# Optimization experiments

Hardware: AMD Instinct MI355X
Metric: run time of the kernel (lower is better)

Reference implementation:

```python
import jax, jax.numpy as jnp
import numpy as np

N_NODES, N_EDGES, N_CRYS = 50000, 1200000, 256
AF, NF, NR = 64, 64, 16
INV_SQRT_2 = 1.0 / 2.0 ** 0.5
EPS = 1e-5


def crystal_norm(x, idx, nseg, gamma, beta):
    # per-crystal, per-feature mean/var normalization
    cnt = jnp.maximum(jax.ops.segment_sum(jnp.ones((x.shape[0],), x.dtype), idx, nseg), 1.0)[:, None]
    mean = jax.ops.segment_sum(x, idx, nseg) / cnt
    d = x - mean[idx]
    var = jax.ops.segment_sum(d * d, idx, nseg) / cnt
    return d / jnp.sqrt(var[idx] + EPS) * gamma + beta


def setup_inputs() -> dict:
    key = jax.random.key(0)
    ks = jax.random.split(key, 16)
    s = 0.05
    return {
        'atom_fea': jax.random.normal(ks[0], (N_NODES, AF), jnp.float32),
        'edge': jax.random.normal(ks[1], (N_EDGES, NF), jnp.float32),
        'rbf': jax.random.uniform(ks[2], (N_EDGES, NR), jnp.float32),
        'nbr_fea_idx': jax.random.randint(ks[3], (N_EDGES, 2), 0, N_NODES),
        'crystal_atom_idx': jax.random.randint(ks[4], (N_NODES,), 0, N_CRYS),
        'crystal_edge_idx': jax.random.randint(ks[5], (N_EDGES,), 0, N_CRYS),
        'W_rbf': jax.random.normal(ks[6], (NR, NF), jnp.float32) * s,
        'W_full': jax.random.normal(ks[7], (2 * AF + NF, 2 * AF), jnp.float32) * s,
        'W_mask': jax.random.normal(ks[8], (AF, 1), jnp.float32) * s,
        'g1': jnp.ones((2 * AF,), jnp.float32),
        'b1': jnp.zeros((2 * AF,), jnp.float32),
        'g2': jnp.ones((AF,), jnp.float32),
        'b2': jnp.zeros((AF,), jnp.float32),
        'Wr1a': jax.random.normal(ks[9], (AF, AF // 2), jnp.float32) * s,
        'Wr1b': jax.random.normal(ks[10], (AF // 2, AF), jnp.float32) * s,
        'Wr2a': jax.random.normal(ks[11], (AF, AF // 2), jnp.float32) * s,
        'Wr2b': jax.random.normal(ks[12], (AF // 2, AF), jnp.float32) * s,
    }


def reference(atom_fea, edge, rbf, nbr_fea_idx, crystal_atom_idx, crystal_edge_idx,
              W_rbf, W_full, W_mask, g1, b1, g2, b2, Wr1a, Wr1b, Wr2a, Wr2b):
    rbf_h = rbf @ W_rbf                                   # [E, NF]
    sum_idx = nbr_fea_idx[:, 0]
    nbr_fea = edge * rbf_h                                # [E, NF]
    atom_nbr_fea = atom_fea[nbr_fea_idx].reshape(-1, 2 * AF)  # [E, 2*AF]
    total = jnp.concatenate([atom_nbr_fea, nbr_fea], axis=1)  # [E, 2*AF+NF]
    gated = total @ W_full                                # [E, 2*AF]
    gated = crystal_norm(gated, crystal_edge_idx, N_CRYS, g1, b1)
    nbr_filter, nbr_core = gated[:, :AF], gated[:, AF:]
    nbr_filter = jax.nn.sigmoid(nbr_filter @ W_mask)      # [E, 1]
    nbr_core = jax.nn.relu(nbr_core)
    msg = nbr_filter * nbr_core                           # [E, AF]
    cnt = jnp.maximum(jax.ops.segment_sum(jnp.ones((msg.shape[0],), msg.dtype), sum_idx, N_NODES), 1.0)[:, None]
    nbr_sumed = jax.ops.segment_sum(msg, sum_idx, N_NODES) / cnt  # scatter-mean
    nbr_sumed = crystal_norm(nbr_sumed, crystal_atom_idx, N_CRYS, g2, b2)
    # 2 residual blocks: out = (x + relu(relu(x W_a) W_b)) / sqrt(2)
    h = jax.nn.relu(jax.nn.relu(nbr_sumed @ Wr1a) @ Wr1b)
    nbr_sumed = (nbr_sumed + h) * INV_SQRT_2
    h = jax.nn.relu(jax.nn.relu(nbr_sumed @ Wr2a) @ Wr2b)
    nbr_sumed = (nbr_sumed + h) * INV_SQRT_2
    return INV_SQRT_2 * jax.nn.relu(atom_fea + nbr_sumed)
```

## Files before the change

### kernel.cpp

```cpp
#include <hip/hip_runtime.h>
#include <hip/hip_bf16.h>

typedef __attribute__((ext_vector_type(8))) short bfrag;
typedef __attribute__((ext_vector_type(4))) float f4;

__device__ __forceinline__ unsigned short f2bf(float f){
  unsigned b = __float_as_uint(f);
  b = (b + 0x7fffu + ((b >> 16) & 1u)) >> 16;
  return (unsigned short)b;
}
__device__ __forceinline__ unsigned pk2bf(float a, float b){
  return (unsigned)f2bf(a) | ((unsigned)f2bf(b) << 16);
}
__device__ __forceinline__ float bf2f(unsigned short u){
  return __uint_as_float(((unsigned)u) << 16);
}
__device__ __forceinline__ bfrag pack8(float4 x, float4 y){
  bfrag r;
  r[0]=(short)f2bf(x.x); r[1]=(short)f2bf(x.y); r[2]=(short)f2bf(x.z); r[3]=(short)f2bf(x.w);
  r[4]=(short)f2bf(y.x); r[5]=(short)f2bf(y.y); r[6]=(short)f2bf(y.z); r[7]=(short)f2bf(y.w);
  return r;
}

__global__ __launch_bounds__(64) void k_prep(const float* __restrict__ Wf, unsigned short* __restrict__ Bpack){
  int l = threadIdx.x; int f = blockIdx.x; int ks = f >> 3; int nt = f & 7;
  int kg = l >> 4; int nn = l & 15;
#pragma unroll
  for (int j = 0; j < 8; ++j){
    int k;
    if (ks < 4) k = ks*32 + kg*8 + j;
    else        k = 128 + (ks-4)*32 + ((j>>2)<<4) + kg*4 + (j&3);
    Bpack[((size_t)f*64 + l)*8 + j] = f2bf(Wf[(size_t)k*128 + nt*16 + nn]);
  }
}

__global__ __launch_bounds__(256) void k_pre(const int* __restrict__ cidxe, int E,
                                             const int* __restrict__ cidxn, int NN,
                                             const int* __restrict__ nbr,
                                             int* __restrict__ ccnte, int* __restrict__ ccntn,
                                             int* __restrict__ ncnt){
  __shared__ int he[256], hn[256];
  int t = threadIdx.x;
  he[t] = 0; hn[t] = 0;
  __syncthreads();
  for (size_t i = (size_t)blockIdx.x*256 + t; i < (size_t)E; i += (size_t)gridDim.x*256){
    atomicAdd(&he[cidxe[i]], 1);
    atomicAdd(&ncnt[nbr[2*i]], 1);
  }
  for (size_t i = (size_t)blockIdx.x*256 + t; i < (size_t)NN; i += (size_t)gridDim.x*256)
    atomicAdd(&hn[cidxn[i]], 1);
  __syncthreads();
  if (he[t]) atomicAdd(&ccnte[t], he[t]);
  if (hn[t]) atomicAdd(&ccntn[t], hn[t]);
}

__global__ __launch_bounds__(1024) void k_scans(const int* __restrict__ ncnt, int NN,
                                                int* __restrict__ offs, int* __restrict__ cursor,
                                                const int* __restrict__ ccnte, const int* __restrict__ ccntn,
                                                int* __restrict__ ceoffs, int* __restrict__ cecur,
                                                int* __restrict__ cnoffs, int* __restrict__ cncur){
  int tid = threadIdx.x;
  if (blockIdx.x == 0){
    __shared__ int part[1024];
    int chunk = (NN + 1023) >> 10;
    int base = tid*chunk;
    int s = 0;
    for (int i = 0; i < chunk; ++i){ int p = base + i; if (p < NN) s += ncnt[p]; }
    part[tid] = s;
    __syncthreads();
    for (int d = 1; d < 1024; d <<= 1){
      int v = (tid >= d) ? part[tid - d] : 0;
      __syncthreads();
      part[tid] += v;
      __syncthreads();
    }
    int run = (tid == 0) ? 0 : part[tid-1];
    for (int i = 0; i < chunk; ++i){
      int p = base + i;
      if (p < NN){ offs[p] = run; cursor[p] = run; run += ncnt[p]; }
    }
    if (tid == 1023) offs[NN] = part[1023];
  } else {
    __shared__ int sh[256];
    const int* cnt = (blockIdx.x == 2) ? ccntn : ccnte;
    int* off = (blockIdx.x == 2) ? cnoffs : ceoffs;
    int* cur = (blockIdx.x == 2) ? cncur  : cecur;
    int v = 0;
    if (tid < 256){ v = cnt[tid]; sh[tid] = v; }
    __syncthreads();
    for (int d = 1; d < 256; d <<= 1){
      int x = (tid >= d && tid < 256) ? sh[tid - d] : 0;
      __syncthreads();
      if (tid < 256) sh[tid] += x;
      __syncthreads();
    }
    if (tid < 256){
      off[tid] = sh[tid] - v; cur[tid] = sh[tid] - v;
      if (tid == 255) off[256] = sh[255];
    }
  }
}

__global__ __launch_bounds__(256) void k_scatter2(const int* __restrict__ nbr, const int* __restrict__ cidxe,
                                                  int E, int* __restrict__ cursor, int4* __restrict__ edat,
                                                  int* __restrict__ gcur, int* __restrict__ celist){
  __shared__ int lhist[256], lbase[256], lcur[256];
  int t = threadIdx.x;
  lhist[t] = 0; lcur[t] = 0;
  __syncthreads();
  int base = blockIdx.x*1024;
  int end = min(base + 1024, E);
  for (int i = base + t; i < end; i += 256) atomicAdd(&lhist[cidxe[i]], 1);
  __syncthreads();
  if (lhist[t]) lbase[t] = atomicAdd(&gcur[t], lhist[t]);
  __syncthreads();
  for (int i = base + t; i < end; i += 256){
    int cr = cidxe[i];
    int n = nbr[2*(size_t)i];
    int j = nbr[2*(size_t)i + 1];
    int pos = atomicAdd(&cursor[n], 1);
    edat[pos] = make_int4(n, j, i, cr);
    int lp = atomicAdd(&lcur[cr], 1);
    celist[lbase[cr] + lp] = pos;
  }
}

__global__ __launch_bounds__(256) void k_cscatter(const int* __restrict__ idx, int n,
                                                  int* __restrict__ gcur, int* __restrict__ outl){
  __shared__ int lhist[256], lbase[256], lcur[256];
  int t = threadIdx.x;
  lhist[t] = 0; lcur[t] = 0;
  __syncthreads();
  int base = blockIdx.x*4096;
  int end = min(base + 4096, n);
  for (int i = base + t; i < end; i += 256) atomicAdd(&lhist[idx[i]], 1);
  __syncthreads();
  if (lhist[t]) lbase[t] = atomicAdd(&gcur[t], lhist[t]);
  __syncthreads();
  for (int i = base + t; i < end; i += 256){
    int b = idx[i];
    int p = atomicAdd(&lcur[b], 1);
    outl[lbase[b] + p] = i;
  }
}

struct TileRegs {
  int ei;
  float4 ra0, ra1, rb0, rb1, rc0, rc1, rd0, rd1, rr0, rr1, re0, re1, re2, re3;
};

__device__ __forceinline__ TileRegs load_tile(const float* __restrict__ atom, const float* __restrict__ edgef,
                                              const float* __restrict__ rbff, const int4* __restrict__ edat,
                                              size_t r0, int e16, int g, int E){
  TileRegs R;
  size_t er = r0 + e16;
  if (er >= (size_t)E) er = 0;
  const int4 ed = edat[er];
  R.ei = ed.z;
  const float4* Ai = (const float4*)(atom + (size_t)ed.x*64);
  const float4* Aj = (const float4*)(atom + (size_t)ed.y*64);
  R.ra0 = Ai[g*2];   R.ra1 = Ai[g*2+1];
  R.rb0 = Ai[8+g*2]; R.rb1 = Ai[8+g*2+1];
  R.rc0 = Aj[g*2];   R.rc1 = Aj[g*2+1];
  R.rd0 = Aj[8+g*2]; R.rd1 = Aj[8+g*2+1];
  R.rr0 = make_float4(0.f,0.f,0.f,0.f);
  R.rr1 = make_float4(0.f,0.f,0.f,0.f);
  if (g < 2){
    const float4* rp = (const float4*)(rbff + (size_t)ed.z*16 + g*8);
    R.rr0 = rp[0]; R.rr1 = rp[1];
  }
  const float4* ep = (const float4*)(edgef + (size_t)ed.z*64);
  R.re0 = ep[g]; R.re1 = ep[4+g]; R.re2 = ep[8+g]; R.re3 = ep[12+g];
  return R;
}

template<int FNT0, int FNT1>
__global__ __launch_bounds__(256) void k_gemm(const float* __restrict__ atom, const float* __restrict__ edgef,
                                              const float* __restrict__ rbff, const int4* __restrict__ edat,
                                              const float* __restrict__ Wrbf,
                                              const unsigned short* __restrict__ Bpack,
                                              unsigned short* __restrict__ gated, int gstride, int colOff,
                                              int nT, int E)
{
  const int lane = threadIdx.x & 63;
  const int wid  = (blockIdx.x*256 + threadIdx.x) >> 6;
  const int nW   = gridDim.x*4;
  const int e16  = lane & 15;
  const int g    = lane >> 4;
  const f4 zero = {0.f, 0.f, 0.f, 0.f};

  bfrag wf[4];
#pragma unroll
  for (int ct = 0; ct < 4; ++ct){
#pragma unroll
    for (int i = 0; i < 8; ++i){
      float v = (g < 2) ? Wrbf[(g*8 + i)*64 + ct*16 + e16] : 0.f;
      wf[ct][i] = (short)f2bf(v);
    }
  }

  size_t t = (size_t)wid;
  if (t >= (size_t)nT) return;
  TileRegs cur = load_tile(atom, edgef, rbff, edat, t*16, e16, g, E);

  while (true){
    const size_t tn = t + (size_t)nW;
    const bool more = tn < (size_t)nT;
    TileRegs nxt;
    if (more) nxt = load_tile(atom, edgef, rbff, edat, tn*16, e16, g, E);

    const size_t r0 = t*16;
    size_t er = r0 + e16;
    const bool rowOK = er < (size_t)E;
    if (!rowOK) er = 0;

    bfrag a[6];
    a[0] = pack8(cur.ra0, cur.ra1);
    a[1] = pack8(cur.rb0, cur.rb1);
    a[2] = pack8(cur.rc0, cur.rc1);
    a[3] = pack8(cur.rd0, cur.rd1);
    bfrag rf = pack8(cur.rr0, cur.rr1);

    f4 h0 = __builtin_amdgcn_mfma_f32_16x16x32_bf16(wf[0], rf, zero, 0, 0, 0);
    f4 h1 = __builtin_amdgcn_mfma_f32_16x16x32_bf16(wf[1], rf, zero, 0, 0, 0);
    f4 h2 = __builtin_amdgcn_mfma_f32_16x16x32_bf16(wf[2], rf, zero, 0, 0, 0);
    f4 h3 = __builtin_amdgcn_mfma_f32_16x16x32_bf16(wf[3], rf, zero, 0, 0, 0);

    const float* pe0 = (const float*)&cur.re0;
    const float* pe1 = (const float*)&cur.re1;
    const float* pe2 = (const float*)&cur.re2;
    const float* pe3 = (const float*)&cur.re3;
#pragma unroll
    for (int r = 0; r < 4; ++r){
      a[4][r]   = (short)f2bf(h0[r]*pe0[r]);
      a[4][4+r] = (short)f2bf(h1[r]*pe1[r]);
      a[5][r]   = (short)f2bf(h2[r]*pe2[r]);
      a[5][4+r] = (short)f2bf(h3[r]*pe3[r]);
    }

    unsigned short* orow = gated + er*(size_t)gstride - colOff;
#pragma unroll
    for (int f_nt = FNT0; f_nt < FNT1; ++f_nt){
      const unsigned short* bb = Bpack + ((size_t)(f_nt*64 + lane))*8;
      f4 acc = zero;
#pragma unroll
      for (int ks = 0; ks < 6; ++ks){
        bfrag b = *(const bfrag*)(bb + (size_t)ks*4096);
        acc = __builtin_amdgcn_mfma_f32_16x16x32_bf16(b, a[ks], acc, 0, 0, 0);
      }
      if (rowOK){
        uint2 pk;
        pk.x = pk2bf(acc[0], acc[1]);
        pk.y = pk2bf(acc[2], acc[3]);
        *(uint2*)(orow + f_nt*16 + g*4) = pk;
      }
    }

    if (!more) break;
    cur = nxt;
    t = tn;
  }
}

__global__ __launch_bounds__(256) void k_cstats128(const unsigned short* __restrict__ gated,
                                                   const int* __restrict__ coffs, const int* __restrict__ celist,
                                                   float* __restrict__ pstat){
  int cr = blockIdx.x >> 3, s = blockIdx.x & 7;
  int t = threadIdx.x, w = t >> 6, lane = t & 63;
  int o0 = coffs[cr], o1 = coffs[cr+1];
  long long L = o1 - o0;
  int lo = o0 + (int)(L*s/8), hi = o0 + (int)(L*(s+1)/8);
  float S0=0.f, Q0=0.f, S1=0.f, Q1=0.f;
  for (int p = lo + w*8; p < hi; p += 32){
#pragma unroll
    for (int u = 0; u < 8; ++u){
      if (p + u < hi){
        int e = celist[p+u];
        unsigned v = *(const unsigned*)(gated + (size_t)e*128 + lane*2);
        float a = bf2f((unsigned short)(v & 0xffffu));
        float b = bf2f((unsigned short)(v >> 16));
        S0 += a; Q0 += a*a; S1 += b; Q1 += b*b;
      }
    }
  }
  __shared__ float sP[4][256];
  sP[w][lane*4+0]=S0; sP[w][lane*4+1]=Q0; sP[w][lane*4+2]=S1; sP[w][lane*4+3]=Q1;
  __syncthreads();
  float v = sP[0][t] + sP[1][t] + sP[2][t] + sP[3][t];
  pstat[((size_t)blockIdx.x << 8) + t] = v;
}

__global__ __launch_bounds__(256) void k_cstats64(const unsigned short* __restrict__ gated,
                                                  const int* __restrict__ coffs, const int* __restrict__ celist,
                                                  float* __restrict__ pstat){
  int cr = blockIdx.x >> 3, s = blockIdx.x & 7;
  int t = threadIdx.x, w = t >> 6, lane = t & 63;
  int o0 = coffs[cr], o1 = coffs[cr+1];
  long long L = o1 - o0;
  int lo = o0 + (int)(L*s/8), hi = o0 + (int)(L*(s+1)/8);
  float S=0.f, Q=0.f;
  for (int p = lo + w*8; p < hi; p += 32){
#pragma unroll
    for (int u = 0; u < 8; ++u){
      if (p + u < hi){
        int e = celist[p+u];
        float a = bf2f(gated[(size_t)e*64 + lane]);
        S += a; Q += a*a;
      }
    }
  }
  __shared__ float sP[4][128];
  sP[w][lane*2+0]=S; sP[w][lane*2+1]=Q;
  __syncthreads();
  if (t < 128){
    float v = sP[0][t] + sP[1][t] + sP[2][t] + sP[3][t];
    pstat[((size_t)blockIdx.x << 7) + t] = v;
  }
}

__global__ __launch_bounds__(256) void k_cnstats(const float* __restrict__ nacc, const int* __restrict__ ncnt,
                                                 const int* __restrict__ coffs, const int* __restrict__ cnlist,
                                                 float* __restrict__ pstat){
  int cr = blockIdx.x >> 1, s = blockIdx.x & 1;
  int t = threadIdx.x, w = t >> 6, lane = t & 63;
  int o0 = coffs[cr], o1 = coffs[cr+1];
  long long L = o1 - o0;
  int lo = o0 + (int)(L*s/2), hi = o0 + (int)(L*(s+1)/2);
  float S=0.f, Q=0.f;
  for (int p = lo + w*4; p < hi; p += 16){
#pragma unroll
    for (int u = 0; u < 4; ++u){
      if (p + u < hi){
        int n = cnlist[p+u];
        float inv = 1.f / fmaxf((float)ncnt[n], 1.f);
        float a = nacc[(size_t)n*64 + lane]*inv;
        S += a; Q += a*a;
      }
    }
  }
  __shared__ float sP[4][128];
  sP[w][lane*2+0]=S; sP[w][lane*2+1]=Q;
  __syncthreads();
  if (t < 128){
    float v = sP[0][t] + sP[1][t] + sP[2][t] + sP[3][t];
    pstat[((size_t)blockIdx.x << 7) + t] = v;
  }
}

__global__ __launch_bounds__(256) void k_red128f(const float* __restrict__ pstat, const int* __restrict__ ccnt,
                                                 const float* __restrict__ gamma, const float* __restrict__ beta,
                                                 const float* __restrict__ Wm,
                                                 float* __restrict__ sc, float* __restrict__ sh,
                                                 float* __restrict__ w2, float* __restrict__ fb){
  int idx = blockIdx.x*256 + threadIdx.x;
  int cr = idx >> 7, col = idx & 127;
  int vS = ((col >> 1) << 2) + ((col & 1) << 1);
  float S=0.f, Q=0.f;
  for (int s2 = 0; s2 < 8; ++s2){
    const float* b = pstat + ((size_t)(cr*8 + s2) << 8);
    S += b[vS]; Q += b[vS+1];
  }
  float cnt = fmaxf((float)ccnt[cr], 1.f);
  float mean = S/cnt;
  float var = fmaxf(Q/cnt - mean*mean, 0.f);
  float r = 1.f / sqrtf(var + 1e-5f);
  float g = r*gamma[col];
  float shv = beta[col] - mean*g;
  sc[cr*128 + col] = g;
  sh[cr*128 + col] = shv;

  __shared__ float red[256];
  float contrib = 0.f;
  if (col < 64){
    float wmv = Wm[col];
    w2[cr*64 + col] = g*wmv;
    contrib = shv*wmv;
  }
  red[threadIdx.x] = contrib;
  __syncthreads();
  int lc = threadIdx.x & 127;
  for (int d = 32; d > 0; d >>= 1){
    if (lc < d) red[threadIdx.x] += red[threadIdx.x + d];
    __syncthreads();
  }
  if (lc == 0) fb[cr] = red[threadIdx.x];
}

__global__ __launch_bounds__(256) void k_red64(const float* __restrict__ pstat, int nsplit,
                                               const int* __restrict__ ccnt,
                                               const float* __restrict__ gamma, const float* __restrict__ beta,
                                               float* __restrict__ sc, float* __restrict__ sh,
                                               int stride, int colOff){
  int idx = blockIdx.x*256 + threadIdx.x;
  int cr = idx >> 6, col = idx & 63;
  int vS = col*2;
  float S=0.f, Q=0.f;
  for (int s2 = 0; s2 < nsplit; ++s2){
    const float* b = pstat + ((size_t)(cr*nsplit + s2) << 7);
    S += b[vS]; Q += b[vS+1];
  }
  float cnt = fmaxf((float)ccnt[cr], 1.f);
  float mean = S/cnt;
  float var = fmaxf(Q/cnt - mean*mean, 0.f);
  float r = 1.f / sqrtf(var + 1e-5f);
  float g = r*gamma[col];
  sc[cr*stride + colOff + col] = g;
  sh[cr*stride + colOff + col] = beta[col] - mean*g;
}

__global__ __launch_bounds__(256) void k_fprep(const float* __restrict__ scE, const float* __restrict__ shE,
                                               const float* __restrict__ Wm, float* __restrict__ w2,
                                               float* __restrict__ fb){
  int t = threadIdx.x, w = t >> 6, lane = t & 63;
  int cr = blockIdx.x*4 + w;
  float wm = Wm[lane];
  w2[cr*64 + lane] = scE[cr*128 + lane]*wm;
  float b = shE[cr*128 + lane]*wm;
#pragma unroll
  for (int d = 1; d < 64; d <<= 1) b += __shfl_xor(b, d, 64);
  if (lane == 0) fb[cr] = b;
}

__global__ __launch_bounds__(256) void k_filter(const unsigned short* __restrict__ gated, int gst,
                                                const int4* __restrict__ edat, const float* __restrict__ w2,
                                                const float* __restrict__ fb, float* __restrict__ filt, int E){
  size_t r = (size_t)blockIdx.x*256 + threadIdx.x;
  if (r >= (size_t)E) return;
  int cr = edat[r].w;
  const uint4* row = (const uint4*)(gated + r*(size_t)gst);
  const float4* wr = (const float4*)(w2 + cr*64);
  float logit = fb[cr];
#pragma unroll
  for (int j = 0; j < 8; ++j){
    uint4 v = row[j];
    float4 wa = wr[2*j], wb = wr[2*j+1];
    logit += bf2f((unsigned short)(v.x & 0xffffu))*wa.x + bf2f((unsigned short)(v.x >> 16))*wa.y;
    logit += bf2f((unsigned short)(v.y & 0xffffu))*wa.z + bf2f((unsigned short)(v.y >> 16))*wa.w;
    logit += bf2f((unsigned short)(v.z & 0xffffu))*wb.x + bf2f((unsigned short)(v.z >> 16))*wb.y;
    logit += bf2f((unsigned short)(v.w & 0xffffu))*wb.z + bf2f((unsigned short)(v.w >> 16))*wb.w;
  }
  filt[r] = 1.f / (1.f + __expf(-logit));
}

__global__ __launch_bounds__(256) void k_msgf8(const unsigned short* __restrict__ gated,
                                               const int4* __restrict__ edat,
                                               const int* __restrict__ offs,
                                               const float* __restrict__ scE, const float* __restrict__ shE,
                                               const float* __restrict__ w2, const float* __restrict__ fb,
                                               float* __restrict__ nacc, int NN){
  int w = threadIdx.x >> 6, lane = threadIdx.x & 63;
  int n = blockIdx.x*4 + w;
  if (n >= NN) return;
  int sub = lane >> 3, c8 = lane & 7;
  float a0=0.f,a1=0.f,a2=0.f,a3=0.f,a4=0.f,a5=0.f,a6=0.f,a7=0.f;
  int p0 = offs[n], p1 = offs[n+1];
  for (int p = p0; p < p1; p += 8){
    int q = p + sub;
    bool ok = q < p1;
    if (!ok) q = p;
    int cr = edat[q].w;
    uint4 vf = *(const uint4*)(gated + (size_t)q*128 + c8*8);
    const float4* wvp = (const float4*)(w2 + cr*64 + c8*8);
    float4 wv0 = wvp[0], wv1 = wvp[1];
    float part = bf2f((unsigned short)(vf.x & 0xffffu))*wv0.x
               + bf2f((unsigned short)(vf.x >> 16))*wv0.y
               + bf2f((unsigned short)(vf.y & 0xffffu))*wv0.z
               + bf2f((unsigned short)(vf.y >> 16))*wv0.w
               + bf2f((unsigned short)(vf.z & 0xffffu))*wv1.x
               + bf2f((unsigned short)(vf.z >> 16))*wv1.y
               + bf2f((unsigned short)(vf.w & 0xffffu))*wv1.z
               + bf2f((unsigned short)(vf.w >> 16))*wv1.w;
#pragma unroll
    for (int d = 1; d < 8; d <<= 1) part += __shfl_xor(part, d, 64);
    float f = 1.f / (1.f + __expf(-(part + fb[cr])));
    uint4 vc = *(const uint4*)(gated + (size_t)q*128 + 64 + c8*8);
    const float4* scp = (const float4*)(scE + cr*128 + 64 + c8*8);
    const float4* shp = (const float4*)(shE + cr*128 + 64 + c8*8);
    float4 s0 = scp[0], s1 = scp[1];
    float4 h0 = shp[0], h1 = shp[1];
    if (ok){
      a0 += f*fmaxf(bf2f((unsigned short)(vc.x & 0xffffu))*s0.x + h0.x, 0.f);
      a1 += f*fmaxf(bf2f((unsigned short)(vc.x >> 16))*s0.y + h0.y, 0.f);
      a2 += f*fmaxf(bf2f((unsigned short)(vc.y & 0xffffu))*s0.z + h0.z, 0.f);
      a3 += f*fmaxf(bf2f((unsigned short)(vc.y >> 16))*s0.w + h0.w, 0.f);
      a4 += f*fmaxf(bf2f((unsigned short)(vc.z & 0xffffu))*s1.x + h1.x, 0.f);
      a5 += f*fmaxf(bf2f((unsigned short)(vc.z >> 16))*s1.y + h1.y, 0.f);
      a6 += f*fmaxf(bf2f((unsigned short)(vc.w & 0xffffu))*s1.z + h1.z, 0.f);
      a7 += f*fmaxf(bf2f((unsigned short)(vc.w >> 16))*s1.w + h1.w, 0.f);
    }
  }
#pragma unroll
  for (int d = 8; d < 64; d <<= 1){
    a0 += __shfl_xor(a0, d, 64); a1 += __shfl_xor(a1, d, 64);
    a2 += __shfl_xor(a2, d, 64); a3 += __shfl_xor(a3, d, 64);
    a4 += __shfl_xor(a4, d, 64); a5 += __shfl_xor(a5, d, 64);
    a6 += __shfl_xor(a6, d, 64); a7 += __shfl_xor(a7, d, 64);
  }
  if (lane < 8){
    float4 o0; o0.x = a0; o0.y = a1; o0.z = a2; o0.w = a3;
    float4 o1; o1.x = a4; o1.y = a5; o1.z = a6; o1.w = a7;
    float4* dst = (float4*)(nacc + (size_t)n*64 + (size_t)c8*8);
    dst[0] = o0; dst[1] = o1;
  }
}

__global__ __launch_bounds__(256) void k_msg3(const unsigned short* __restrict__ gated, int gst, int colBase,
                                              const int4* __restrict__ edat, const float* __restrict__ filt,
                                              const int* __restrict__ offs,
                                              const float* __restrict__ scE, const float* __restrict__ shE,
                                              int scOff, float* __restrict__ nacc, int NN){
  int w = threadIdx.x >> 6, lane = threadIdx.x & 63;
  int n = blockIdx.x*4 + w;
  if (n >= NN) return;
  int sub = lane >> 5, c2 = lane & 31;
  float a0 = 0.f, a1 = 0.f;
  int p0 = offs[n], p1 = offs[n+1];
  for (int p = p0; p < p1; p += 2){
    int idx = p + sub;
    bool ok = idx < p1;
    int q = ok ? idx : p;
    unsigned v = *(const unsigned*)(gated + (size_t)q*gst + colBase + c2*2);
    float f = filt[q];
    int cr = edat[q].w;
    float2 sc2 = *(const float2*)(scE + cr*128 + scOff + c2*2);
    float2 sh2 = *(const float2*)(shE + cr*128 + scOff + c2*2);
    if (ok){
      float g0 = bf2f((unsigned short)(v & 0xffffu));
      float g1 = bf2f((unsigned short)(v >> 16));
      a0 += f*fmaxf(g0*sc2.x + sh2.x, 0.f);
      a1 += f*fmaxf(g1*sc2.y + sh2.y, 0.f);
    }
  }
  a0 += __shfl_xor(a0, 32, 64);
  a1 += __shfl_xor(a1, 32, 64);
  if (lane < 32) *(float2*)(nacc + (size_t)n*64 + (size_t)c2*2) = make_float2(a0, a1);
}

__global__ __launch_bounds__(256) void k_final(const float* __restrict__ nacc, const int* __restrict__ ncnt,
                                               const int* __restrict__ cidx, const float* __restrict__ nsc,
                                               const float* __restrict__ nsh, const float* __restrict__ W1a,
                                               const float* __restrict__ W1b, const float* __restrict__ W2a,
                                               const float* __restrict__ W2b, const float* __restrict__ atom,
                                               float* __restrict__ out, int NN)
{
  __shared__ float sW[4][2048];
  __shared__ float hbuf[8192];
  int tid = threadIdx.x;
  for (int i = tid; i < 2048; i += 256){
    sW[0][i] = W1a[i]; sW[1][i] = W1b[i]; sW[2][i] = W2a[i]; sW[3][i] = W2b[i];
  }
  __syncthreads();
  int n = blockIdx.x*256 + tid;
  if (n >= NN) return;
  const float ISQ2 = 0.70710678118654752440f;
  int cr = cidx[n];
  float inv = 1.f / fmaxf((float)ncnt[n], 1.f);
  float x[64];
  const float4* src = (const float4*)(nacc + (size_t)n*64);
#pragma unroll
  for (int j = 0; j < 16; ++j){
    float4 v = src[j];
    x[4*j] = v.x*inv; x[4*j+1] = v.y*inv; x[4*j+2] = v.z*inv; x[4*j+3] = v.w*inv;
  }
#pragma unroll
  for (int c = 0; c < 64; ++c)
    x[c] = x[c]*nsc[cr*64 + c] + nsh[cr*64 + c];

  for (int blk = 0; blk < 2; ++blk){
    const float* sa = sW[blk*2];
    const float* sb = sW[blk*2 + 1];
    for (int j = 0; j < 32; ++j){
      float s = 0.f;
#pragma unroll
      for (int k = 0; k < 64; ++k) s += x[k]*sa[k*32 + j];
      hbuf[tid*32 + (j ^ (tid & 31))] = fmaxf(s, 0.f);
    }
    float x2[64];
#pragma unroll
    for (int c = 0; c < 64; ++c) x2[c] = 0.f;
    for (int j = 0; j < 32; ++j){
      float hj = hbuf[tid*32 + (j ^ (tid & 31))];
#pragma unroll
      for (int c = 0; c < 64; ++c) x2[c] += hj*sb[j*64 + c];
    }
#pragma unroll
    for (int c = 0; c < 64; ++c)
      x[c] = (x[c] + fmaxf(x2[c], 0.f))*ISQ2;
  }
  const float4* ap = (const float4*)(atom + (size_t)n*64);
  float4* op = (float4*)(out + (size_t)n*64);
#pragma unroll
  for (int j = 0; j < 16; ++j){
    float4 av = ap[j]; float4 o;
    o.x = ISQ2*fmaxf(av.x + x[4*j],   0.f);
    o.y = ISQ2*fmaxf(av.y + x[4*j+1], 0.f);
    o.z = ISQ2*fmaxf(av.z + x[4*j+2], 0.f);
    o.w = ISQ2*fmaxf(av.w + x[4*j+3], 0.f);
    op[j] = o;
  }
}

extern "C" void kernel_launch(void* const* d_in, const int* in_sizes, int n_in,
                              void* d_out, int out_size, void* d_ws, size_t ws_size,
                              hipStream_t stream)
{
  const float* atom  = (const float*)d_in[0];
  const float* edgef = (const float*)d_in[1];
  const float* rbff  = (const float*)d_in[2];
  const int*   nbr   = (const int*)d_in[3];
  const int*   cidxn = (const int*)d_in[4];
  const int*   cidxe = (const int*)d_in[5];
  const float* Wrbf  = (const float*)d_in[6];
  const float* Wful  = (const float*)d_in[7];
  const float* Wmask = (const float*)d_in[8];
  const float* g1    = (const float*)d_in[9];
  const float* b1    = (const float*)d_in[10];
  const float* g2    = (const float*)d_in[11];
  const float* b2    = (const float*)d_in[12];
  const float* W1a   = (const float*)d_in[13];
  const float* W1b   = (const float*)d_in[14];
  const float* W2a   = (const float*)d_in[15];
  const float* W2b   = (const float*)d_in[16];
  float* out = (float*)d_out;

  const int E  = in_sizes[1] / 64;
  const int NN = in_sizes[0] / 64;
  const int nT = (E + 15) / 16;

  char* p = (char*)d_ws;
  auto take = [&](size_t bytes){ void* r = (void*)p; p += (bytes + 255) & ~(size_t)255; return r; };

  const bool full = ws_size >= (size_t)360000000;
  const int gstride = full ? 128 : 64;

  unsigned short* gated = (unsigned short*)take((size_t)E*gstride*2);
  float* pstat  = (float*)take((size_t)2048*256*4);
  float* pstatN = (float*)take((size_t)512*128*4);
  float* nacc   = (float*)take((size_t)NN*64*4);
  int*   ncnt   = (int*)take((size_t)NN*4);
  int*   offs   = (int*)take((size_t)(NN+1)*4);
  int*   cursor = (int*)take((size_t)NN*4);
  int4*  edat   = (int4*)take((size_t)E*16);
  int*   celist = (int*)take((size_t)E*4);
  int*   cnlist = (int*)take((size_t)NN*4);
  int*   ceoffs = (int*)take(257*4);
  int*   cecur  = (int*)take(256*4);
  int*   cnoffs = (int*)take(257*4);
  int*   cncur  = (int*)take(256*4);
  int*   ccnte  = (int*)take(1024);
  int*   ccntn  = (int*)take(1024);
  float* scE    = (float*)take(256*128*4);
  float* shE    = (float*)take(256*128*4);
  float* nsc    = (float*)take(256*64*4);
  float* nsh    = (float*)take(256*64*4);
  float* w2     = (float*)take(256*64*4);
  float* fb     = (float*)take(256*4);
  float* filt   = (float*)take((size_t)E*4);
  unsigned short* Bpack = (unsigned short*)take(6*8*64*8*2);

  (void)hipMemsetAsync(ncnt,  0, (size_t)NN*4, stream);
  (void)hipMemsetAsync(ccnte, 0, 1024, stream);
  (void)hipMemsetAsync(ccntn, 0, 1024, stream);

  k_prep<<<48, 64, 0, stream>>>(Wful, Bpack);
  k_pre<<<2048, 256, 0, stream>>>(cidxe, E, cidxn, NN, nbr, ccnte, ccntn, ncnt);
  k_scans<<<3, 1024, 0, stream>>>(ncnt, NN, offs, cursor, ccnte, ccntn, ceoffs, cecur, cnoffs, cncur);
  k_scatter2<<<(E + 1023)/1024, 256, 0, stream>>>(nbr, cidxe, E, cursor, edat, cecur, celist);
  k_cscatter<<<(NN + 4095)/4096, 256, 0, stream>>>(cidxn, NN, cncur, cnlist);

  if (full){
    k_gemm<0,8><<<2048, 256, 0, stream>>>(atom, edgef, rbff, edat, Wrbf, Bpack, gated, 128, 0, nT, E);
    k_cstats128<<<2048, 256, 0, stream>>>(gated, ceoffs, celist, pstat);
    k_red128f<<<128, 256, 0, stream>>>(pstat, ccnte, g1, b1, Wmask, scE, shE, w2, fb);
    k_msgf8<<<(NN + 3)/4, 256, 0, stream>>>(gated, edat, offs, scE, shE, w2, fb, nacc, NN);
  } else {
    k_gemm<0,4><<<2048, 256, 0, stream>>>(atom, edgef, rbff, edat, Wrbf, Bpack, gated, 64, 0, nT, E);
    k_cstats64<<<2048, 256, 0, stream>>>(gated, ceoffs, celist, pstat);
    k_red64<<<64, 256, 0, stream>>>(pstat, 8, ccnte, g1, b1, scE, shE, 128, 0);
    k_fprep<<<64, 256, 0, stream>>>(scE, shE, Wmask, w2, fb);
    k_filter<<<(E + 255)/256, 256, 0, stream>>>(gated, 64, edat, w2, fb, filt, E);
    k_gemm<4,8><<<2048, 256, 0, stream>>>(atom, edgef, rbff, edat, Wrbf, Bpack, gated, 64, 64, nT, E);
    k_cstats64<<<2048, 256, 0, stream>>>(gated, ceoffs, celist, pstat);
    k_red64<<<64, 256, 0, stream>>>(pstat, 8, ccnte, g1 + 64, b1 + 64, scE, shE, 128, 64);
    k_msg3<<<(NN + 3)/4, 256, 0, stream>>>(gated, 64, 0, edat, filt, offs, scE, shE, 64, nacc, NN);
  }

  k_cnstats<<<512, 256, 0, stream>>>(nacc, ncnt, cnoffs, cnlist, pstatN);
  k_red64<<<64, 256, 0, stream>>>(pstatN, 2, ccntn, g2, b2, nsc, nsh, 64, 0);
  k_final<<<(NN + 255)/256, 256, 0, stream>>>(nacc, ncnt, cidxn, nsc, nsh, W1a, W1b, W2a, W2b, atom, out, NN);
}
```

Measured before the change: 952.8 us.

## Store gated in original edge order and stage packed weights in LDS

```diff
diff --git a/kernel.cpp b/kernel.cpp
--- a/kernel.cpp
+++ b/kernel.cpp
@@ -121,7 +121,7 @@
     int pos = atomicAdd(&cursor[n], 1);
     edat[pos] = make_int4(n, j, i, cr);
     int lp = atomicAdd(&lcur[cr], 1);
-    celist[lbase[cr] + lp] = pos;
+    celist[lbase[cr] + lp] = i;
   }
 }
 
@@ -145,20 +145,18 @@
 }
 
 struct TileRegs {
-  int ei;
   float4 ra0, ra1, rb0, rb1, rc0, rc1, rd0, rd1, rr0, rr1, re0, re1, re2, re3;
 };
 
 __device__ __forceinline__ TileRegs load_tile(const float* __restrict__ atom, const float* __restrict__ edgef,
-                                              const float* __restrict__ rbff, const int4* __restrict__ edat,
+                                              const float* __restrict__ rbff, const int* __restrict__ nbr,
                                               size_t r0, int e16, int g, int E){
   TileRegs R;
-  size_t er = r0 + e16;
-  if (er >= (size_t)E) er = 0;
-  const int4 ed = edat[er];
-  R.ei = ed.z;
-  const float4* Ai = (const float4*)(atom + (size_t)ed.x*64);
-  const float4* Aj = (const float4*)(atom + (size_t)ed.y*64);
+  size_t e = r0 + e16;
+  if (e >= (size_t)E) e = 0;
+  int2 nn = *(const int2*)(nbr + 2*e);
+  const float4* Ai = (const float4*)(atom + (size_t)nn.x*64);
+  const float4* Aj = (const float4*)(atom + (size_t)nn.y*64);
   R.ra0 = Ai[g*2];   R.ra1 = Ai[g*2+1];
   R.rb0 = Ai[8+g*2]; R.rb1 = Ai[8+g*2+1];
   R.rc0 = Aj[g*2];   R.rc1 = Aj[g*2+1];
@@ -166,22 +164,24 @@
   R.rr0 = make_float4(0.f,0.f,0.f,0.f);
   R.rr1 = make_float4(0.f,0.f,0.f,0.f);
   if (g < 2){
-    const float4* rp = (const float4*)(rbff + (size_t)ed.z*16 + g*8);
+    const float4* rp = (const float4*)(rbff + e*16 + g*8);
     R.rr0 = rp[0]; R.rr1 = rp[1];
   }
-  const float4* ep = (const float4*)(edgef + (size_t)ed.z*64);
+  const float4* ep = (const float4*)(edgef + e*64);
   R.re0 = ep[g]; R.re1 = ep[4+g]; R.re2 = ep[8+g]; R.re3 = ep[12+g];
   return R;
 }
 
 template<int FNT0, int FNT1>
 __global__ __launch_bounds__(256) void k_gemm(const float* __restrict__ atom, const float* __restrict__ edgef,
-                                              const float* __restrict__ rbff, const int4* __restrict__ edat,
+                                              const float* __restrict__ rbff, const int* __restrict__ nbr,
                                               const float* __restrict__ Wrbf,
                                               const unsigned short* __restrict__ Bpack,
                                               unsigned short* __restrict__ gated, int gstride, int colOff,
                                               int nT, int E)
 {
+  __shared__ uint4 sBv[3072];
+  const unsigned short* sB = (const unsigned short*)sBv;
   const int lane = threadIdx.x & 63;
   const int wid  = (blockIdx.x*256 + threadIdx.x) >> 6;
   const int nW   = gridDim.x*4;
@@ -189,6 +189,11 @@
   const int g    = lane >> 4;
   const f4 zero = {0.f, 0.f, 0.f, 0.f};
 
+  {
+    const uint4* src = (const uint4*)Bpack;
+    for (int i = threadIdx.x; i < 3072; i += 256) sBv[i] = src[i];
+  }
+
   bfrag wf[4];
 #pragma unroll
   for (int ct = 0; ct < 4; ++ct){
@@ -198,21 +203,22 @@
       wf[ct][i] = (short)f2bf(v);
     }
   }
+  __syncthreads();
 
   size_t t = (size_t)wid;
   if (t >= (size_t)nT) return;
-  TileRegs cur = load_tile(atom, edgef, rbff, edat, t*16, e16, g, E);
+  TileRegs cur = load_tile(atom, edgef, rbff, nbr, t*16, e16, g, E);
 
   while (true){
     const size_t tn = t + (size_t)nW;
     const bool more = tn < (size_t)nT;
     TileRegs nxt;
-    if (more) nxt = load_tile(atom, edgef, rbff, edat, tn*16, e16, g, E);
+    if (more) nxt = load_tile(atom, edgef, rbff, nbr, tn*16, e16, g, E);
 
     const size_t r0 = t*16;
-    size_t er = r0 + e16;
-    const bool rowOK = er < (size_t)E;
-    if (!rowOK) er = 0;
+    size_t e = r0 + e16;
+    const bool rowOK = e < (size_t)E;
+    if (!rowOK) e = 0;
 
     bfrag a[6];
     a[0] = pack8(cur.ra0, cur.ra1);
@@ -238,14 +244,14 @@
       a[5][4+r] = (short)f2bf(h3[r]*pe3[r]);
     }
 
-    unsigned short* orow = gated + er*(size_t)gstride - colOff;
+    unsigned short* orow = gated + e*(size_t)gstride - colOff;
 #pragma unroll
     for (int f_nt = FNT0; f_nt < FNT1; ++f_nt){
-      const unsigned short* bb = Bpack + ((size_t)(f_nt*64 + lane))*8;
+      const unsigned short* bls = sB + ((size_t)(f_nt*64 + lane))*8;
       f4 acc = zero;
 #pragma unroll
       for (int ks = 0; ks < 6; ++ks){
-        bfrag b = *(const bfrag*)(bb + (size_t)ks*4096);
+        bfrag b = *(const bfrag*)(bls + (size_t)ks*4096);
         acc = __builtin_amdgcn_mfma_f32_16x16x32_bf16(b, a[ks], acc, 0, 0, 0);
       }
       if (rowOK){
@@ -426,8 +432,9 @@
                                                 const float* __restrict__ fb, float* __restrict__ filt, int E){
   size_t r = (size_t)blockIdx.x*256 + threadIdx.x;
   if (r >= (size_t)E) return;
-  int cr = edat[r].w;
-  const uint4* row = (const uint4*)(gated + r*(size_t)gst);
+  int4 ed = edat[r];
+  int cr = ed.w;
+  const uint4* row = (const uint4*)(gated + (size_t)ed.z*(size_t)gst);
   const float4* wr = (const float4*)(w2 + cr*64);
   float logit = fb[cr];
 #pragma unroll
@@ -458,8 +465,10 @@
     int q = p + sub;
     bool ok = q < p1;
     if (!ok) q = p;
-    int cr = edat[q].w;
-    uint4 vf = *(const uint4*)(gated + (size_t)q*128 + c8*8);
+    int4 ed = edat[q];
+    int cr = ed.w;
+    size_t row = (size_t)ed.z*128;
+    uint4 vf = *(const uint4*)(gated + row + c8*8);
     const float4* wvp = (const float4*)(w2 + cr*64 + c8*8);
     float4 wv0 = wvp[0], wv1 = wvp[1];
     float part = bf2f((unsigned short)(vf.x & 0xffffu))*wv0.x
@@ -473,7 +482,7 @@
 #pragma unroll
     for (int d = 1; d < 8; d <<= 1) part += __shfl_xor(part, d, 64);
     float f = 1.f / (1.f + __expf(-(part + fb[cr])));
-    uint4 vc = *(const uint4*)(gated + (size_t)q*128 + 64 + c8*8);
+    uint4 vc = *(const uint4*)(gated + row + 64 + c8*8);
     const float4* scp = (const float4*)(scE + cr*128 + 64 + c8*8);
     const float4* shp = (const float4*)(shE + cr*128 + 64 + c8*8);
     float4 s0 = scp[0], s1 = scp[1];
@@ -519,9 +528,10 @@
     int idx = p + sub;
     bool ok = idx < p1;
     int q = ok ? idx : p;
-    unsigned v = *(const unsigned*)(gated + (size_t)q*gst + colBase + c2*2);
+    int4 ed = edat[q];
+    unsigned v = *(const unsigned*)(gated + (size_t)ed.z*gst + colBase + c2*2);
     float f = filt[q];
-    int cr = edat[q].w;
+    int cr = ed.w;
     float2 sc2 = *(const float2*)(scE + cr*128 + scOff + c2*2);
     float2 sh2 = *(const float2*)(shE + cr*128 + scOff + c2*2);
     if (ok){
@@ -669,17 +679,17 @@
   k_cscatter<<<(NN + 4095)/4096, 256, 0, stream>>>(cidxn, NN, cncur, cnlist);
 
   if (full){
-    k_gemm<0,8><<<2048, 256, 0, stream>>>(atom, edgef, rbff, edat, Wrbf, Bpack, gated, 128, 0, nT, E);
+    k_gemm<0,8><<<2048, 256, 0, stream>>>(atom, edgef, rbff, nbr, Wrbf, Bpack, gated, 128, 0, nT, E);
     k_cstats128<<<2048, 256, 0, stream>>>(gated, ceoffs, celist, pstat);
     k_red128f<<<128, 256, 0, stream>>>(pstat, ccnte, g1, b1, Wmask, scE, shE, w2, fb);
     k_msgf8<<<(NN + 3)/4, 256, 0, stream>>>(gated, edat, offs, scE, shE, w2, fb, nacc, NN);
   } else {
-    k_gemm<0,4><<<2048, 256, 0, stream>>>(atom, edgef, rbff, edat, Wrbf, Bpack, gated, 64, 0, nT, E);
+    k_gemm<0,4><<<2048, 256, 0, stream>>>(atom, edgef, rbff, nbr, Wrbf, Bpack, gated, 64, 0, nT, E);
     k_cstats64<<<2048, 256, 0, stream>>>(gated, ceoffs, celist, pstat);
     k_red64<<<64, 256, 0, stream>>>(pstat, 8, ccnte, g1, b1, scE, shE, 128, 0);
     k_fprep<<<64, 256, 0, stream>>>(scE, shE, Wmask, w2, fb);
     k_filter<<<(E + 255)/256, 256, 0, stream>>>(gated, 64, edat, w2, fb, filt, E);
-    k_gemm<4,8><<<2048, 256, 0, stream>>>(atom, edgef, rbff, edat, Wrbf, Bpack, gated, 64, 64, nT, E);
+    k_gemm<4,8><<<2048, 256, 0, stream>>>(atom, edgef, rbff, nbr, Wrbf, Bpack, gated, 64, 64, nT, E);
     k_cstats64<<<2048, 256, 0, stream>>>(gated, ceoffs, celist, pstat);
     k_red64<<<64, 256, 0, stream>>>(pstat, 8, ccnte, g1 + 64, b1 + 64, scE, shE, 128, 64);
     k_msg3<<<(NN + 3)/4, 256, 0, stream>>>(gated, 64, 0, edat, filt, offs, scE, shE, 64, nacc, NN);
```

Result: slower. 978.3 us (+2.7%).
